# Kernel optimization log

Hardware: AMD Instinct MI355X
Metric: run time of the kernel (lower is better)

Reference implementation:

```python
import jax, jax.numpy as jnp
import numpy as np

RCR, RCA = 5.2, 3.5
ETA_R, ZETA, ETA_A = 16.0, 32.0, 8.0
SHF_R = 0.9 + 0.26875 * np.arange(16)            # 16 radial shifts
SHF_Z = (2.0 * np.arange(8) + 1.0) * np.pi / 16.0  # 8 angular shifts
SHF_A = 0.9 + 0.65 * np.arange(4)                # 4 angular-radial shifts
NUM_SPECIES = 4
_pm = np.zeros((NUM_SPECIES, NUM_SPECIES), np.int32)
_c = 0
for _s1 in range(NUM_SPECIES):
    for _s2 in range(_s1, NUM_SPECIES):
        _pm[_s1, _s2] = _pm[_s2, _s1] = _c
        _c += 1
PAIR_IDX = _pm  # unordered species pair -> 0..9 (torchani triu order)


def setup_inputs():
    key = jax.random.key(0)
    k1, k2 = jax.random.split(key)
    B, N = 512, 16
    species = jax.random.randint(k1, (B, N), 0, NUM_SPECIES)
    coordinates = jax.random.normal(k2, (B, N, 3), dtype=jnp.float32) * 2.0
    return {"species": species, "coordinates": coordinates}


def _aev(species, coordinates):
    B, N, _ = coordinates.shape
    dt = coordinates.dtype
    shfr = jnp.asarray(SHF_R, dt)
    shfz = jnp.asarray(SHF_Z, dt)
    shfa = jnp.asarray(SHF_A, dt)
    valid = species >= 0                                   # padding atoms have species = -1
    eye = jnp.eye(N, dtype=bool)
    pair_valid = valid[:, :, None] & valid[:, None, :] & ~eye          # [B,N,N]
    diff = coordinates[:, :, None, :] - coordinates[:, None, :, :]     # [B,N,N,3]
    d2 = jnp.sum(diff * diff, axis=-1)
    d = jnp.sqrt(jnp.where(pair_valid, d2, 1.0))                       # safe distances
    sp1h = jax.nn.one_hot(species, NUM_SPECIES, dtype=dt)              # [B,N,4]; zeros for padding

    # ---- radial AEV (cutoff Rcr) ----
    fcr = jnp.where(pair_valid & (d <= RCR), 0.5 * jnp.cos(jnp.pi * d / RCR) + 0.5, 0.0)
    rad = 0.25 * jnp.exp(-ETA_R * (d[..., None] - shfr) ** 2) * fcr[..., None]   # [B,N,N,16]
    radial_aev = jnp.einsum('bijr,bjs->bisr', rad, sp1h).reshape(B, N, NUM_SPECIES * 16)

    # ---- angular AEV (cutoff Rca) ----
    fca = jnp.where(pair_valid & (d <= RCA), 0.5 * jnp.cos(jnp.pi * d / RCA) + 0.5, 0.0)
    dot = jnp.einsum('bijx,bikx->bijk', diff, diff)                    # [B,N,N,N]
    cosang = jnp.clip(0.95 * dot / (d[:, :, :, None] * d[:, :, None, :]), -0.95, 0.95)
    ang = jnp.arccos(cosang)                                           # [B,N,N,N]
    f1 = ((1.0 + jnp.cos(ang[..., None] - shfz)) * 0.5) ** ZETA        # [B,N,N,N,8]
    davg = 0.5 * (d[:, :, :, None] + d[:, :, None, :])
    f2 = jnp.exp(-ETA_A * (davg[..., None] - shfa) ** 2)               # [B,N,N,N,4]
    tri = (fca[:, :, :, None] * fca[:, :, None, :]) * (~eye).astype(dt)[None, None]  # j != k
    # torchani subaev layout flattens (ShfA, ShfZ) -> 4*8 = 32
    ret = (tri[..., None, None] * f2[..., :, None] * f1[..., None, :]).reshape(B, N, N, N, 32)
    pair_oh = jax.nn.one_hot(jnp.asarray(PAIR_IDX), 10, dtype=dt)      # [4,4,10]
    w = jnp.einsum('bjs,bkt,stp->bjkp', sp1h, sp1h, pair_oh)           # [B,N,N,10]
    # torchani: 2*f1*f2*fc per UNORDERED pair; here ordered (j,k) double-counts -> net factor 1
    angular_aev = jnp.einsum('bijkf,bjkp->bipf', ret, w).reshape(B, N, 10 * 32)
    return jnp.concatenate([radial_aev, angular_aev], axis=-1)         # [B,N,384]


def reference(species, coordinates):
    return species, _aev(species, coordinates)
```

## Files before the change

kernel.cpp:

```cpp
#include <hip/hip_runtime.h>

__global__ __launch_bounds__(256, 8) void aev_kernel(const int* __restrict__ species,
                                                     const float* __restrict__ coords,
                                                     float* __restrict__ out,
                                                     int nmol) {
    const int t = threadIdx.x;
    const int w = t >> 6;
    const int l = t & 63;
    const int bid = blockIdx.x;
    const int b = bid >> 2;
    const int g = bid & 3;
    const int i = g * 4 + w;

    __shared__ float  scm[4][48];
    __shared__ int    ssp[4][16];
    __shared__ float4 pd[4][16];
    __shared__ float4 pf[4][16];
    __shared__ float  rad[4][16][17];
    __shared__ int    vlist[4][16];
    __shared__ int    hist[4][10], sBase[4][10], sCur[4][10];
    __shared__ float4 ebuf[4][105];

    if (l < 48) scm[w][l] = coords[b * 48 + l];
    if (l < 16) {
        int sp = species[b * 16 + l];
        ssp[w][l] = sp;
        if (g == 0 && w == 0) out[b * 16 + l] = (float)sp;
    }
    if (l < 10) hist[w][l] = 0;

    const int f = l & 31, z = f & 7, a = f >> 3;
    const float ang = (2.0f * (float)z + 1.0f) * 0.19634954084936207f;
    const float czh = 0.5f * __cosf(ang);
    const float szh = 0.5f * __sinf(ang);
    const float ga  = __expf(-3.38f * (float)(a * a - a));

    const int spi = ssp[w][i];
    const float xi = scm[w][3 * i], yi = scm[w][3 * i + 1], zi = scm[w][3 * i + 2];

    int  spl = 0;
    bool pvalid = false;
    if (l < 16) {
        spl = ssp[w][l];
        float dx = xi - scm[w][3 * l], dy = yi - scm[w][3 * l + 1], dz = zi - scm[w][3 * l + 2];
        bool pv = (l != i) && (spi >= 0) && (spl >= 0);
        float d2 = dx * dx + dy * dy + dz * dz;
        float d2s = pv ? d2 : 1.0f;
        float rinv = __frsqrt_rn(d2s);
        float d = d2s * rinv;
        float fca  = (pv && d <= 3.5f) ? fmaf(0.5f, __cosf(d * 0.8975979010256552f), 0.5f) : 0.0f;
        float fcr4 = (pv && d <= 5.2f) ? 0.25f * fmaf(0.5f, __cosf(d * 0.6041515809446141f), 0.5f) : 0.0f;
        pd[w][l] = make_float4(dx, dy, dz, d);
        pf[w][l] = make_float4(rinv, fca, fcr4, 0.0f);
        pvalid = fca > 0.0f;
    }
    const unsigned long long vm = __ballot(pvalid);
    const int V = __popcll(vm);
    if (pvalid) {
        int idx = __popcll(vm & ((1ull << l) - 1ull));
        vlist[w][idx] = l | (spl << 4);
    }
    const unsigned m0 = (unsigned)__ballot(l < 16 && spl == 0);
    const unsigned m1 = (unsigned)__ballot(l < 16 && spl == 1);
    const unsigned m2 = (unsigned)__ballot(l < 16 && spl == 2);
    const unsigned m3 = (unsigned)__ballot(l < 16 && spl == 3);

    {
        const int jj = l & 15, rg = l >> 4;
        float d = pd[w][jj].w;
        float fcr4 = pf[w][jj].z;
        #pragma unroll
        for (int rr = 0; rr < 4; ++rr) {
            int r = rg * 4 + rr;
            float e = d - (0.9f + 0.26875f * (float)r);
            rad[w][jj][r] = fcr4 * __expf(-16.0f * e * e);
        }
    }

    const int nt = (V * (V - 1)) >> 1;
    const int tw = 2 * V - 1;
    float ca0 = 0.f, sa0 = 0.f, t00 = 0.f, r10 = 0.f; int p0 = -1;
    float ca1 = 0.f, sa1 = 0.f, t01 = 0.f, r11 = 0.f; int p1 = -1;
    #pragma unroll
    for (int slot = 0; slot < 2; ++slot) {
        const int s = slot == 0 ? l : (64 + l);
        if (s < nt) {
            float disc = (float)(tw * tw - 8 * s);
            int aa = (int)floorf(0.5f * ((float)tw - sqrtf(disc)));
            aa = aa < 0 ? 0 : (aa > V - 2 ? V - 2 : aa);
            int offa = (aa * (2 * V - 1 - aa)) >> 1;
            if (s < offa) { --aa; offa = (aa * (2 * V - 1 - aa)) >> 1; }
            else { int offn = ((aa + 1) * (2 * V - 2 - aa)) >> 1; if (s >= offn) { ++aa; offa = offn; } }
            const int bb = aa + 1 + (s - offa);
            const int va = vlist[w][aa], vb = vlist[w][bb];
            const int j = va & 15, spj = va >> 4;
            const int k = vb & 15, spk = vb >> 4;
            float4 Pj = pd[w][j], Pk = pd[w][k];
            float4 Fj = pf[w][j], Fk = pf[w][k];
            float dot = Pj.x * Pk.x + Pj.y * Pk.y + Pj.z * Pk.z;
            float ca = 0.95f * dot * Fj.x * Fk.x;
            ca = fminf(0.95f, fmaxf(-0.95f, ca));
            float s2 = 1.0f - ca * ca;
            float sa = s2 * __frsqrt_rn(s2);
            float davg = 0.5f * (Pj.w + Pk.w);
            float e0 = davg - 0.9f;
            float t0 = 2.0f * Fj.y * Fk.y * __expf(-8.0f * e0 * e0);
            float r1 = __expf(10.4f * davg - 12.74f);
            int lo = spj < spk ? spj : spk, hi = spj < spk ? spk : spj;
            int p = lo * 4 + hi - ((lo * (lo + 1)) >> 1);
            atomicAdd(&hist[w][p], 1);
            if (slot == 0) { ca0 = ca; sa0 = sa; t00 = t0; r10 = r1; p0 = p; }
            else           { ca1 = ca; sa1 = sa; t01 = t0; r11 = r1; p1 = p; }
        }
    }

    if (l < 10) {
        int sum = 0;
        for (int qq = 0; qq < l; ++qq) sum += hist[w][qq];
        sBase[w][l] = sum;
        sCur[w][l] = sum;
    }

    if (p0 >= 0) { int idx = atomicAdd(&sCur[w][p0], 1); ebuf[w][idx] = make_float4(ca0, sa0, t00, r10); }
    if (p1 >= 0) { int idx = atomicAdd(&sCur[w][p1], 1); ebuf[w][idx] = make_float4(ca1, sa1, t01, r11); }

    float* base_o = out + (size_t)nmol * 16 + (size_t)(b * 16 + i) * 384;
    {
        const int half = l >> 5;
        const bool a1 = (a & 1), a2 = (a & 2) != 0;
        #pragma unroll
        for (int pp = 0; pp < 5; ++pp) {
            int p = pp * 2 + half;
            int st = sBase[w][p];
            int n = hist[w][p];
            float acc = 0.0f;
            for (int e = 0; e < n; ++e) {
                float4 v = ebuf[w][st + e];
                float c1 = fmaf(czh, v.x, fmaf(szh, v.y, 0.5f));
                float c2 = c1 * c1;
                float c4 = c2 * c2;
                float c8 = c4 * c4;
                float c16 = c8 * c8;
                float c32 = c16 * c16;
                float tt = v.z;
                float rsq = v.w * v.w;
                tt = a1 ? tt * v.w : tt;
                tt = a2 ? tt * rsq : tt;
                acc = fmaf(tt, c32, acc);
            }
            base_o[64 + p * 32 + f] = acc * ga;
        }
    }

    {
        const int s_ = l >> 4, r_ = l & 15;
        unsigned m = s_ < 2 ? (s_ == 0 ? m0 : m1) : (s_ == 2 ? m2 : m3);
        float rv = 0.0f;
        while (m) {
            int jj = __ffs(m) - 1;
            m &= m - 1;
            rv += rad[w][jj][r_];
        }
        base_o[l] = rv;
    }
}

extern "C" void kernel_launch(void* const* d_in, const int* in_sizes, int n_in,
                              void* d_out, int out_size, void* d_ws, size_t ws_size,
                              hipStream_t stream) {
    const int*   species = (const int*)d_in[0];
    const float* coords  = (const float*)d_in[1];
    float*       out     = (float*)d_out;
    int nmol = in_sizes[0] / 16;
    aev_kernel<<<nmol * 4, 256, 0, stream>>>(species, coords, out, nmol);
}
```

Measured before the change: 68.09 us.

## Map one central atom per half-wavefront, halving the grid size

Each 64-lane wavefront now handles two central atoms, one per 32-lane half, instead of one atom per wavefront. Each block covers 8 atoms, so the grid drops to two blocks per molecule. Per-atom work (triplet slots, radial shifts, pair outputs) is spread over 32 lanes with more iterations per lane. The aim is to use the lanes that sat idle in the old one-atom-per-wave mapping and to cut the block count. In exchange there is more serial work per lane, higher register use (launch bounds lowered to 4), and more shared memory per block.

```diff
diff --git a/kernel.cpp b/kernel.cpp
--- a/kernel.cpp
+++ b/kernel.cpp
@@ -1,25 +1,27 @@
 #include <hip/hip_runtime.h>
 
-__global__ __launch_bounds__(256, 8) void aev_kernel(const int* __restrict__ species,
+__global__ __launch_bounds__(256, 4) void aev_kernel(const int* __restrict__ species,
                                                      const float* __restrict__ coords,
                                                      float* __restrict__ out,
                                                      int nmol) {
-    const int t = threadIdx.x;
-    const int w = t >> 6;
-    const int l = t & 63;
-    const int bid = blockIdx.x;
-    const int b = bid >> 2;
-    const int g = bid & 3;
-    const int i = g * 4 + w;
+    const int t  = threadIdx.x;
+    const int w  = t >> 6;
+    const int l  = t & 63;
+    const int h  = l >> 5;
+    const int lh = l & 31;
+    const int cb = w * 2 + h;
+    const int b  = blockIdx.x >> 1;
+    const int g  = blockIdx.x & 1;
+    const int i  = g * 8 + cb;
 
     __shared__ float  scm[4][48];
     __shared__ int    ssp[4][16];
-    __shared__ float4 pd[4][16];
-    __shared__ float4 pf[4][16];
-    __shared__ float  rad[4][16][17];
-    __shared__ int    vlist[4][16];
-    __shared__ int    hist[4][10], sBase[4][10], sCur[4][10];
-    __shared__ float4 ebuf[4][105];
+    __shared__ float4 pd[8][16];
+    __shared__ float4 pf[8][16];
+    __shared__ float  rad[8][16][17];
+    __shared__ int    vlist[8][16];
+    __shared__ int    hist[8][10], sBase[8][10], sCur[8][10];
+    __shared__ float4 ebuf[8][105];
 
     if (l < 48) scm[w][l] = coords[b * 48 + l];
     if (l < 16) {
@@ -27,9 +29,9 @@
         ssp[w][l] = sp;
         if (g == 0 && w == 0) out[b * 16 + l] = (float)sp;
     }
-    if (l < 10) hist[w][l] = 0;
+    if (lh < 10) hist[cb][lh] = 0;
 
-    const int f = l & 31, z = f & 7, a = f >> 3;
+    const int z = lh & 7, a = lh >> 3;
     const float ang = (2.0f * (float)z + 1.0f) * 0.19634954084936207f;
     const float czh = 0.5f * __cosf(ang);
     const float szh = 0.5f * __sinf(ang);
@@ -40,50 +42,56 @@
 
     int  spl = 0;
     bool pvalid = false;
-    if (l < 16) {
-        spl = ssp[w][l];
-        float dx = xi - scm[w][3 * l], dy = yi - scm[w][3 * l + 1], dz = zi - scm[w][3 * l + 2];
-        bool pv = (l != i) && (spi >= 0) && (spl >= 0);
+    if (lh < 16) {
+        spl = ssp[w][lh];
+        float dx = xi - scm[w][3 * lh], dy = yi - scm[w][3 * lh + 1], dz = zi - scm[w][3 * lh + 2];
+        bool pv = (lh != i) && (spi >= 0) && (spl >= 0);
         float d2 = dx * dx + dy * dy + dz * dz;
         float d2s = pv ? d2 : 1.0f;
         float rinv = __frsqrt_rn(d2s);
         float d = d2s * rinv;
         float fca  = (pv && d <= 3.5f) ? fmaf(0.5f, __cosf(d * 0.8975979010256552f), 0.5f) : 0.0f;
         float fcr4 = (pv && d <= 5.2f) ? 0.25f * fmaf(0.5f, __cosf(d * 0.6041515809446141f), 0.5f) : 0.0f;
-        pd[w][l] = make_float4(dx, dy, dz, d);
-        pf[w][l] = make_float4(rinv, fca, fcr4, 0.0f);
+        pd[cb][lh] = make_float4(dx, dy, dz, d);
+        pf[cb][lh] = make_float4(rinv, fca, fcr4, 0.0f);
         pvalid = fca > 0.0f;
     }
     const unsigned long long vm = __ballot(pvalid);
-    const int V = __popcll(vm);
+    const unsigned vmh = (unsigned)((vm >> (32 * h)) & 0xFFFFull);
+    const int V = __popc(vmh);
     if (pvalid) {
-        int idx = __popcll(vm & ((1ull << l) - 1ull));
-        vlist[w][idx] = l | (spl << 4);
+        int idx = __popc(vmh & ((1u << lh) - 1u));
+        vlist[cb][idx] = lh | (spl << 4);
     }
-    const unsigned m0 = (unsigned)__ballot(l < 16 && spl == 0);
-    const unsigned m1 = (unsigned)__ballot(l < 16 && spl == 1);
-    const unsigned m2 = (unsigned)__ballot(l < 16 && spl == 2);
-    const unsigned m3 = (unsigned)__ballot(l < 16 && spl == 3);
+    const unsigned long long b0 = __ballot(lh < 16 && spl == 0);
+    const unsigned long long b1 = __ballot(lh < 16 && spl == 1);
+    const unsigned long long b2 = __ballot(lh < 16 && spl == 2);
+    const unsigned long long b3 = __ballot(lh < 16 && spl == 3);
+    const unsigned sm0 = (unsigned)((b0 >> (32 * h)) & 0xFFFFull);
+    const unsigned sm1 = (unsigned)((b1 >> (32 * h)) & 0xFFFFull);
+    const unsigned sm2 = (unsigned)((b2 >> (32 * h)) & 0xFFFFull);
+    const unsigned sm3 = (unsigned)((b3 >> (32 * h)) & 0xFFFFull);
 
     {
-        const int jj = l & 15, rg = l >> 4;
-        float d = pd[w][jj].w;
-        float fcr4 = pf[w][jj].z;
+        const int jj = lh & 15, rg = lh >> 4;
+        float d = pd[cb][jj].w;
+        float fcr4 = pf[cb][jj].z;
         #pragma unroll
-        for (int rr = 0; rr < 4; ++rr) {
-            int r = rg * 4 + rr;
+        for (int rr = 0; rr < 8; ++rr) {
+            int r = rg * 8 + rr;
             float e = d - (0.9f + 0.26875f * (float)r);
-            rad[w][jj][r] = fcr4 * __expf(-16.0f * e * e);
+            rad[cb][jj][r] = fcr4 * __expf(-16.0f * e * e);
         }
     }
 
     const int nt = (V * (V - 1)) >> 1;
     const int tw = 2 * V - 1;
-    float ca0 = 0.f, sa0 = 0.f, t00 = 0.f, r10 = 0.f; int p0 = -1;
-    float ca1 = 0.f, sa1 = 0.f, t01 = 0.f, r11 = 0.f; int p1 = -1;
+    float caS[4], saS[4], t0S[4], r1S[4];
+    int pS[4];
     #pragma unroll
-    for (int slot = 0; slot < 2; ++slot) {
-        const int s = slot == 0 ? l : (64 + l);
+    for (int slot = 0; slot < 4; ++slot) {
+        pS[slot] = -1;
+        const int s = slot * 32 + lh;
         if (s < nt) {
             float disc = (float)(tw * tw - 8 * s);
             int aa = (int)floorf(0.5f * ((float)tw - sqrtf(disc)));
@@ -92,11 +100,11 @@
             if (s < offa) { --aa; offa = (aa * (2 * V - 1 - aa)) >> 1; }
             else { int offn = ((aa + 1) * (2 * V - 2 - aa)) >> 1; if (s >= offn) { ++aa; offa = offn; } }
             const int bb = aa + 1 + (s - offa);
-            const int va = vlist[w][aa], vb = vlist[w][bb];
+            const int va = vlist[cb][aa], vb = vlist[cb][bb];
             const int j = va & 15, spj = va >> 4;
             const int k = vb & 15, spk = vb >> 4;
-            float4 Pj = pd[w][j], Pk = pd[w][k];
-            float4 Fj = pf[w][j], Fk = pf[w][k];
+            float4 Pj = pd[cb][j], Pk = pd[cb][k];
+            float4 Fj = pf[cb][j], Fk = pf[cb][k];
             float dot = Pj.x * Pk.x + Pj.y * Pk.y + Pj.z * Pk.z;
             float ca = 0.95f * dot * Fj.x * Fk.x;
             ca = fminf(0.95f, fmaxf(-0.95f, ca));
@@ -108,34 +116,36 @@
             float r1 = __expf(10.4f * davg - 12.74f);
             int lo = spj < spk ? spj : spk, hi = spj < spk ? spk : spj;
             int p = lo * 4 + hi - ((lo * (lo + 1)) >> 1);
-            atomicAdd(&hist[w][p], 1);
-            if (slot == 0) { ca0 = ca; sa0 = sa; t00 = t0; r10 = r1; p0 = p; }
-            else           { ca1 = ca; sa1 = sa; t01 = t0; r11 = r1; p1 = p; }
+            atomicAdd(&hist[cb][p], 1);
+            caS[slot] = ca; saS[slot] = sa; t0S[slot] = t0; r1S[slot] = r1; pS[slot] = p;
         }
     }
 
-    if (l < 10) {
+    if (lh < 10) {
         int sum = 0;
-        for (int qq = 0; qq < l; ++qq) sum += hist[w][qq];
-        sBase[w][l] = sum;
-        sCur[w][l] = sum;
+        for (int qq = 0; qq < lh; ++qq) sum += hist[cb][qq];
+        sBase[cb][lh] = sum;
+        sCur[cb][lh] = sum;
     }
 
-    if (p0 >= 0) { int idx = atomicAdd(&sCur[w][p0], 1); ebuf[w][idx] = make_float4(ca0, sa0, t00, r10); }
-    if (p1 >= 0) { int idx = atomicAdd(&sCur[w][p1], 1); ebuf[w][idx] = make_float4(ca1, sa1, t01, r11); }
+    #pragma unroll
+    for (int slot = 0; slot < 4; ++slot) {
+        if (pS[slot] >= 0) {
+            int idx = atomicAdd(&sCur[cb][pS[slot]], 1);
+            ebuf[cb][idx] = make_float4(caS[slot], saS[slot], t0S[slot], r1S[slot]);
+        }
+    }
 
     float* base_o = out + (size_t)nmol * 16 + (size_t)(b * 16 + i) * 384;
     {
-        const int half = l >> 5;
         const bool a1 = (a & 1), a2 = (a & 2) != 0;
         #pragma unroll
-        for (int pp = 0; pp < 5; ++pp) {
-            int p = pp * 2 + half;
-            int st = sBase[w][p];
-            int n = hist[w][p];
+        for (int p = 0; p < 10; ++p) {
+            int st = sBase[cb][p];
+            int n = hist[cb][p];
             float acc = 0.0f;
             for (int e = 0; e < n; ++e) {
-                float4 v = ebuf[w][st + e];
+                float4 v = ebuf[cb][st + e];
                 float c1 = fmaf(czh, v.x, fmaf(szh, v.y, 0.5f));
                 float c2 = c1 * c1;
                 float c4 = c2 * c2;
@@ -148,20 +158,21 @@
                 tt = a2 ? tt * rsq : tt;
                 acc = fmaf(tt, c32, acc);
             }
-            base_o[64 + p * 32 + f] = acc * ga;
+            base_o[64 + p * 32 + lh] = acc * ga;
         }
     }
 
-    {
-        const int s_ = l >> 4, r_ = l & 15;
-        unsigned m = s_ < 2 ? (s_ == 0 ? m0 : m1) : (s_ == 2 ? m2 : m3);
+    #pragma unroll
+    for (int pass = 0; pass < 2; ++pass) {
+        const int s_ = pass * 2 + (lh >> 4), r_ = lh & 15;
+        unsigned m = s_ < 2 ? (s_ == 0 ? sm0 : sm1) : (s_ == 2 ? sm2 : sm3);
         float rv = 0.0f;
         while (m) {
             int jj = __ffs(m) - 1;
             m &= m - 1;
-            rv += rad[w][jj][r_];
+            rv += rad[cb][jj][r_];
         }
-        base_o[l] = rv;
+        base_o[s_ * 16 + r_] = rv;
     }
 }
 
@@ -172,5 +183,5 @@
     const float* coords  = (const float*)d_in[1];
     float*       out     = (float*)d_out;
     int nmol = in_sizes[0] / 16;
-    aev_kernel<<<nmol * 4, 256, 0, stream>>>(species, coords, out, nmol);
+    aev_kernel<<<nmol * 2, 256, 0, stream>>>(species, coords, out, nmol);
 }
```

Measured after the change: 67.96 us. No clear change (-0.2%).
